# Optimization experiments

Measured on AMD Instinct MI355X. Metric: run time of the kernel, lower is better.

Reference implementation:

```python
import jax, jax.numpy as jnp
import numpy as np

N_NODES = 200000
D_FEAT = 128
B = 40000
DEG = 16
E = B * DEG
D_OUT = 256
N_CLASSES = 128


def setup_inputs() -> dict:
    key = jax.random.key(0)
    ks = jax.random.split(key, 8)
    inputs = jax.random.randint(ks[0], (B,), 0, N_NODES)
    neighbor_ids = jax.random.randint(ks[1], (E,), 0, N_NODES)
    segment_ids = jnp.repeat(jnp.arange(B, dtype=jnp.int64 if jax.config.jax_enable_x64 else jnp.int32), DEG)
    feat_data = jax.random.normal(ks[2], (N_NODES, D_FEAT), dtype=jnp.float32)
    W1 = jax.random.normal(ks[3], (D_OUT, 2 * D_FEAT), dtype=jnp.float32) * 0.05
    b1 = jax.random.normal(ks[4], (D_OUT,), dtype=jnp.float32) * 0.05
    W3 = jax.random.normal(ks[5], (N_CLASSES, D_OUT), dtype=jnp.float32) * 0.05
    b3 = jax.random.normal(ks[6], (N_CLASSES,), dtype=jnp.float32) * 0.05
    return {"inputs": inputs, "neighbor_ids": neighbor_ids, "segment_ids": segment_ids,
            "feat_data": feat_data, "W1": W1, "b1": b1, "W3": W3, "b3": b3}


def reference(inputs, neighbor_ids, segment_ids, feat_data, W1, b1, W3, b3):
    # Segment-mean over neighbor features (replaces Python per-node loop)
    neigh = feat_data[neighbor_ids]                               # [E, D]
    sums = jax.ops.segment_sum(neigh, segment_ids, num_segments=B)  # [B, D]
    cnt = jax.ops.segment_sum(jnp.ones((E,), jnp.float32), segment_ids, num_segments=B)
    means = sums / jnp.maximum(cnt, 1.0)[:, None]                 # [B, D]
    # Concat self + neighbor-mean, linear1
    emb = jnp.concatenate([feat_data[inputs], means], axis=1)     # [B, 2D]
    h = emb @ W1.T + b1                                           # [B, D_OUT]
    # ReLU -> linear3 -> L2 normalize (F.normalize, eps=1e-12)
    logits = jax.nn.relu(h) @ W3.T + b3                           # [B, n_classes]
    norm = jnp.linalg.norm(logits, axis=1, keepdims=True)
    return logits / jnp.maximum(norm, 1e-12)
```

## Files before the change

### kernel.cpp

```cpp
#include <hip/hip_runtime.h>
#include <stdint.h>

#define NNODES 200000
#define BNODES 40000
#define DEG    16
#define DFEAT  128
#define DOUT   256
#define NCLS   128
#define TILE   32

typedef __attribute__((ext_vector_type(8))) __bf16 bf16x8;
typedef __attribute__((ext_vector_type(4))) float  floatx4;

__device__ __forceinline__ uint32_t f2bf(float f) {
  uint32_t x = __float_as_uint(f);
  return ((x + 0x7fffu + ((x >> 16) & 1u)) >> 16) & 0xffffu;
}

__global__ void cvt_weights(const float* __restrict__ W1, const float* __restrict__ W3,
                            uint16_t* __restrict__ w1b, uint16_t* __restrict__ w3b) {
  int i = blockIdx.x * 256 + threadIdx.x;
  if (i < DOUT * 2 * DFEAT) w1b[i] = (uint16_t)f2bf(W1[i]);
  if (i < NCLS * DOUT)      w3b[i] = (uint16_t)f2bf(W3[i]);
}

__global__ __launch_bounds__(256) void sage_fused(
    const int* __restrict__ inputs, const int* __restrict__ nbr,
    const float* __restrict__ feat,
    const uint16_t* __restrict__ w1b, const float* __restrict__ b1,
    const uint16_t* __restrict__ w3b, const float* __restrict__ b3,
    float* __restrict__ out) {
  __shared__ __align__(16) uint16_t embL[TILE][264];
  __shared__ __align__(16) uint16_t hL[TILE][264];
  __shared__ __align__(16) float    lgL[TILE][132];

  const int tid  = threadIdx.x;
  const int w    = tid >> 6;
  const int lane = tid & 63;
  const int quad = lane >> 4;
  const int l16  = lane & 15;

  {
    const int nodeBase = blockIdx.x * TILE + w * 8;
#pragma unroll
    for (int n = 0; n < 8; ++n) {
      const int node = nodeBase + n;
      const int row  = w * 8 + n;
      const int* nb  = nbr + node * DEG;
      float sx = 0.f, sy = 0.f;
#pragma unroll
      for (int j = 0; j < DEG; ++j) {
        const float2 v = *(const float2*)(feat + (size_t)nb[j] * DFEAT + lane * 2);
        sx += v.x; sy += v.y;
      }
      const float2 sv = *(const float2*)(feat + (size_t)inputs[node] * DFEAT + lane * 2);
      const uint32_t selfp = f2bf(sv.x) | (f2bf(sv.y) << 16);
      const uint32_t meanp = f2bf(sx * 0.0625f) | (f2bf(sy * 0.0625f) << 16);
      *(uint32_t*)&embL[row][lane * 2]         = selfp;
      *(uint32_t*)&embL[row][DFEAT + lane * 2] = meanp;
    }
  }
  __syncthreads();

  const int kq = quad * 8;

  {
    floatx4 acc[2][4];
#pragma unroll
    for (int mt = 0; mt < 2; ++mt)
#pragma unroll
      for (int ot = 0; ot < 4; ++ot) {
        floatx4 z = {0.f, 0.f, 0.f, 0.f};
        acc[mt][ot] = z;
      }
#pragma unroll
    for (int kt = 0; kt < 8; ++kt) {
      const int k0 = kt * 32 + kq;
      const bf16x8 a0 = *(const bf16x8*)&embL[l16][k0];
      const bf16x8 a1 = *(const bf16x8*)&embL[16 + l16][k0];
#pragma unroll
      for (int ot = 0; ot < 4; ++ot) {
        const int o = (w * 4 + ot) * 16 + l16;
        const bf16x8 b = *(const bf16x8*)(w1b + o * 256 + k0);
        acc[0][ot] = __builtin_amdgcn_mfma_f32_16x16x32_bf16(a0, b, acc[0][ot], 0, 0, 0);
        acc[1][ot] = __builtin_amdgcn_mfma_f32_16x16x32_bf16(a1, b, acc[1][ot], 0, 0, 0);
      }
    }
#pragma unroll
    for (int ot = 0; ot < 4; ++ot) {
      const int o = (w * 4 + ot) * 16 + l16;
      const float bias = b1[o];
#pragma unroll
      for (int mt = 0; mt < 2; ++mt)
#pragma unroll
        for (int r = 0; r < 4; ++r) {
          float v = acc[mt][ot][r] + bias;
          v = fmaxf(v, 0.f);
          hL[mt * 16 + quad * 4 + r][o] = (uint16_t)f2bf(v);
        }
    }
  }
  __syncthreads();

  {
    floatx4 acc2[2][2];
#pragma unroll
    for (int mt = 0; mt < 2; ++mt)
#pragma unroll
      for (int ct = 0; ct < 2; ++ct) {
        floatx4 z = {0.f, 0.f, 0.f, 0.f};
        acc2[mt][ct] = z;
      }
#pragma unroll
    for (int kt = 0; kt < 8; ++kt) {
      const int k0 = kt * 32 + kq;
      const bf16x8 a0 = *(const bf16x8*)&hL[l16][k0];
      const bf16x8 a1 = *(const bf16x8*)&hL[16 + l16][k0];
#pragma unroll
      for (int ct = 0; ct < 2; ++ct) {
        const int c = (w * 2 + ct) * 16 + l16;
        const bf16x8 b = *(const bf16x8*)(w3b + c * 256 + k0);
        acc2[0][ct] = __builtin_amdgcn_mfma_f32_16x16x32_bf16(a0, b, acc2[0][ct], 0, 0, 0);
        acc2[1][ct] = __builtin_amdgcn_mfma_f32_16x16x32_bf16(a1, b, acc2[1][ct], 0, 0, 0);
      }
    }
#pragma unroll
    for (int ct = 0; ct < 2; ++ct) {
      const int c = (w * 2 + ct) * 16 + l16;
      const float bias = b3[c];
#pragma unroll
      for (int mt = 0; mt < 2; ++mt)
#pragma unroll
        for (int r = 0; r < 4; ++r)
          lgL[mt * 16 + quad * 4 + r][c] = acc2[mt][ct][r] + bias;
    }
  }
  __syncthreads();

  {
    const int nr  = tid >> 3;
    const int sub = tid & 7;
    const float* lrow = &lgL[nr][sub * 16];
    float4 v0 = *(const float4*)(lrow + 0);
    float4 v1 = *(const float4*)(lrow + 4);
    float4 v2 = *(const float4*)(lrow + 8);
    float4 v3 = *(const float4*)(lrow + 12);
    float ss = v0.x * v0.x + v0.y * v0.y + v0.z * v0.z + v0.w * v0.w
             + v1.x * v1.x + v1.y * v1.y + v1.z * v1.z + v1.w * v1.w
             + v2.x * v2.x + v2.y * v2.y + v2.z * v2.z + v2.w * v2.w
             + v3.x * v3.x + v3.y * v3.y + v3.z * v3.z + v3.w * v3.w;
    ss += __shfl_xor(ss, 1);
    ss += __shfl_xor(ss, 2);
    ss += __shfl_xor(ss, 4);
    const float scale = 1.f / fmaxf(sqrtf(ss), 1e-12f);
    v0.x *= scale; v0.y *= scale; v0.z *= scale; v0.w *= scale;
    v1.x *= scale; v1.y *= scale; v1.z *= scale; v1.w *= scale;
    v2.x *= scale; v2.y *= scale; v2.z *= scale; v2.w *= scale;
    v3.x *= scale; v3.y *= scale; v3.z *= scale; v3.w *= scale;
    float* op = out + ((size_t)(blockIdx.x * TILE + nr)) * NCLS + sub * 16;
    *(float4*)(op + 0)  = v0;
    *(float4*)(op + 4)  = v1;
    *(float4*)(op + 8)  = v2;
    *(float4*)(op + 12) = v3;
  }
}

extern "C" void kernel_launch(void* const* d_in, const int* in_sizes, int n_in,
                              void* d_out, int out_size, void* d_ws, size_t ws_size,
                              hipStream_t stream) {
  const int*   inputs = (const int*)d_in[0];
  const int*   nbr    = (const int*)d_in[1];
  const float* feat   = (const float*)d_in[3];
  const float* W1     = (const float*)d_in[4];
  const float* b1     = (const float*)d_in[5];
  const float* W3     = (const float*)d_in[6];
  const float* b3     = (const float*)d_in[7];

  uint16_t* w1b = (uint16_t*)d_ws;
  uint16_t* w3b = w1b + DOUT * 2 * DFEAT;

  cvt_weights<<<(DOUT * 2 * DFEAT) / 256, 256, 0, stream>>>(W1, W3, w1b, w3b);
  sage_fused<<<BNODES / TILE, 256, 0, stream>>>(inputs, nbr, feat, w1b, b1, w3b, b3,
                                                (float*)d_out);
}
```

Before: 218.0 us.

## Alias LDS buffers, widen gather loads to float4, raise occupancy hint

The embedding and logits staging buffers now share one LDS union, guarded by an extra barrier, which shrinks shared memory per block. The neighbor gather now uses float4 loads, with each half-wavefront handling alternate neighbors and a cross-half shuffle to combine the sums. Self features are loaded in a separate float4 pass. A launch-bounds hint of four blocks per CU is added so more waves stay resident to hide gather latency, at the cost of an extra barrier and possible register pressure.

```diff
diff --git a/kernel.cpp b/kernel.cpp
--- a/kernel.cpp
+++ b/kernel.cpp
@@ -24,15 +24,17 @@
   if (i < NCLS * DOUT)      w3b[i] = (uint16_t)f2bf(W3[i]);
 }
 
-__global__ __launch_bounds__(256) void sage_fused(
+__global__ __launch_bounds__(256, 4) void sage_fused(
     const int* __restrict__ inputs, const int* __restrict__ nbr,
     const float* __restrict__ feat,
     const uint16_t* __restrict__ w1b, const float* __restrict__ b1,
     const uint16_t* __restrict__ w3b, const float* __restrict__ b3,
     float* __restrict__ out) {
-  __shared__ __align__(16) uint16_t embL[TILE][264];
+  __shared__ __align__(16) union {
+    uint16_t emb[TILE][264];
+    float    lg[TILE][132];
+  } u0;
   __shared__ __align__(16) uint16_t hL[TILE][264];
-  __shared__ __align__(16) float    lgL[TILE][132];
 
   const int tid  = threadIdx.x;
   const int w    = tid >> 6;
@@ -41,23 +43,46 @@
   const int l16  = lane & 15;
 
   {
+    const int half = lane >> 5;
+    const int hl   = lane & 31;
     const int nodeBase = blockIdx.x * TILE + w * 8;
+
+#pragma unroll
+    for (int p = 0; p < 4; ++p) {
+      const int n0   = 2 * p + half;
+      const int node = nodeBase + n0;
+      const int row  = w * 8 + n0;
+      const float4 v = *(const float4*)(feat + (size_t)inputs[node] * DFEAT + hl * 4);
+      uint2 pk;
+      pk.x = f2bf(v.x) | (f2bf(v.y) << 16);
+      pk.y = f2bf(v.z) | (f2bf(v.w) << 16);
+      *(uint2*)&u0.emb[row][hl * 4] = pk;
+    }
+
 #pragma unroll
     for (int n = 0; n < 8; ++n) {
       const int node = nodeBase + n;
       const int row  = w * 8 + n;
       const int* nb  = nbr + node * DEG;
-      float sx = 0.f, sy = 0.f;
-#pragma unroll
-      for (int j = 0; j < DEG; ++j) {
-        const float2 v = *(const float2*)(feat + (size_t)nb[j] * DFEAT + lane * 2);
-        sx += v.x; sy += v.y;
-      }
-      const float2 sv = *(const float2*)(feat + (size_t)inputs[node] * DFEAT + lane * 2);
-      const uint32_t selfp = f2bf(sv.x) | (f2bf(sv.y) << 16);
-      const uint32_t meanp = f2bf(sx * 0.0625f) | (f2bf(sy * 0.0625f) << 16);
-      *(uint32_t*)&embL[row][lane * 2]         = selfp;
-      *(uint32_t*)&embL[row][DFEAT + lane * 2] = meanp;
+      float4 a = {0.f, 0.f, 0.f, 0.f};
+#pragma unroll
+      for (int j = 0; j < 8; ++j) {
+        const int i0 = nb[2 * j];
+        const int i1 = nb[2 * j + 1];
+        const int idx = half ? i1 : i0;
+        const float4 v = *(const float4*)(feat + (size_t)idx * DFEAT + hl * 4);
+        a.x += v.x; a.y += v.y; a.z += v.z; a.w += v.w;
+      }
+      a.x += __shfl_xor(a.x, 32);
+      a.y += __shfl_xor(a.y, 32);
+      a.z += __shfl_xor(a.z, 32);
+      a.w += __shfl_xor(a.w, 32);
+      if (half == 0) {
+        uint2 pk;
+        pk.x = f2bf(a.x * 0.0625f) | (f2bf(a.y * 0.0625f) << 16);
+        pk.y = f2bf(a.z * 0.0625f) | (f2bf(a.w * 0.0625f) << 16);
+        *(uint2*)&u0.emb[row][DFEAT + hl * 4] = pk;
+      }
     }
   }
   __syncthreads();
@@ -76,8 +101,8 @@
 #pragma unroll
     for (int kt = 0; kt < 8; ++kt) {
       const int k0 = kt * 32 + kq;
-      const bf16x8 a0 = *(const bf16x8*)&embL[l16][k0];
-      const bf16x8 a1 = *(const bf16x8*)&embL[16 + l16][k0];
+      const bf16x8 a0 = *(const bf16x8*)&u0.emb[l16][k0];
+      const bf16x8 a1 = *(const bf16x8*)&u0.emb[16 + l16][k0];
 #pragma unroll
       for (int ot = 0; ot < 4; ++ot) {
         const int o = (w * 4 + ot) * 16 + l16;
@@ -124,6 +149,7 @@
         acc2[1][ct] = __builtin_amdgcn_mfma_f32_16x16x32_bf16(a1, b, acc2[1][ct], 0, 0, 0);
       }
     }
+    __syncthreads();
 #pragma unroll
     for (int ct = 0; ct < 2; ++ct) {
       const int c = (w * 2 + ct) * 16 + l16;
@@ -132,7 +158,7 @@
       for (int mt = 0; mt < 2; ++mt)
 #pragma unroll
         for (int r = 0; r < 4; ++r)
-          lgL[mt * 16 + quad * 4 + r][c] = acc2[mt][ct][r] + bias;
+          u0.lg[mt * 16 + quad * 4 + r][c] = acc2[mt][ct][r] + bias;
     }
   }
   __syncthreads();
@@ -140,7 +166,7 @@
   {
     const int nr  = tid >> 3;
     const int sub = tid & 7;
-    const float* lrow = &lgL[nr][sub * 16];
+    const float* lrow = &u0.lg[nr][sub * 16];
     float4 v0 = *(const float4*)(lrow + 0);
     float4 v1 = *(const float4*)(lrow + 4);
     float4 v2 = *(const float4*)(lrow + 8);
```

New measurement: 218.7 us. About the same (+0.3%).

## Interleave neighbor gathers across nodes and alias logits LDS with embedding buffer

Applied to the files above, without the earlier changes.

The gather loop is reordered so each wave issues loads for all 8 nodes at each neighbor index, and self features are loaded up front. This raises the number of independent global loads in flight and so hides gather latency better. The logits buffer now shares LDS with the embedding buffer through a union, with an extra barrier before the write. That cuts shared memory per block, which may allow more blocks per CU, at the cost of more live registers and one more sync.

```diff
diff --git a/kernel.cpp b/kernel.cpp
--- a/kernel.cpp
+++ b/kernel.cpp
@@ -30,9 +30,11 @@
     const uint16_t* __restrict__ w1b, const float* __restrict__ b1,
     const uint16_t* __restrict__ w3b, const float* __restrict__ b3,
     float* __restrict__ out) {
-  __shared__ __align__(16) uint16_t embL[TILE][264];
+  __shared__ __align__(16) union {
+    uint16_t emb[TILE][264];
+    float    lg[TILE][132];
+  } u0;
   __shared__ __align__(16) uint16_t hL[TILE][264];
-  __shared__ __align__(16) float    lgL[TILE][132];
 
   const int tid  = threadIdx.x;
   const int w    = tid >> 6;
@@ -42,22 +44,33 @@
 
   {
     const int nodeBase = blockIdx.x * TILE + w * 8;
+    const int* nbp = nbr + nodeBase * DEG;
+
+    float2 sv[8];
+#pragma unroll
+    for (int n = 0; n < 8; ++n)
+      sv[n] = *(const float2*)(feat + (size_t)inputs[nodeBase + n] * DFEAT + lane * 2);
+
+    float2 acc[8];
+#pragma unroll
+    for (int n = 0; n < 8; ++n) { acc[n].x = 0.f; acc[n].y = 0.f; }
+
+#pragma unroll
+    for (int j = 0; j < DEG; ++j) {
+#pragma unroll
+      for (int n = 0; n < 8; ++n) {
+        const int idx = nbp[n * DEG + j];
+        const float2 v = *(const float2*)(feat + (size_t)idx * DFEAT + lane * 2);
+        acc[n].x += v.x; acc[n].y += v.y;
+      }
+    }
+
 #pragma unroll
     for (int n = 0; n < 8; ++n) {
-      const int node = nodeBase + n;
-      const int row  = w * 8 + n;
-      const int* nb  = nbr + node * DEG;
-      float sx = 0.f, sy = 0.f;
-#pragma unroll
-      for (int j = 0; j < DEG; ++j) {
-        const float2 v = *(const float2*)(feat + (size_t)nb[j] * DFEAT + lane * 2);
-        sx += v.x; sy += v.y;
-      }
-      const float2 sv = *(const float2*)(feat + (size_t)inputs[node] * DFEAT + lane * 2);
-      const uint32_t selfp = f2bf(sv.x) | (f2bf(sv.y) << 16);
-      const uint32_t meanp = f2bf(sx * 0.0625f) | (f2bf(sy * 0.0625f) << 16);
-      *(uint32_t*)&embL[row][lane * 2]         = selfp;
-      *(uint32_t*)&embL[row][DFEAT + lane * 2] = meanp;
+      const int row = w * 8 + n;
+      *(uint32_t*)&u0.emb[row][lane * 2] = f2bf(sv[n].x) | (f2bf(sv[n].y) << 16);
+      *(uint32_t*)&u0.emb[row][DFEAT + lane * 2] =
+          f2bf(acc[n].x * 0.0625f) | (f2bf(acc[n].y * 0.0625f) << 16);
     }
   }
   __syncthreads();
@@ -76,8 +89,8 @@
 #pragma unroll
     for (int kt = 0; kt < 8; ++kt) {
       const int k0 = kt * 32 + kq;
-      const bf16x8 a0 = *(const bf16x8*)&embL[l16][k0];
-      const bf16x8 a1 = *(const bf16x8*)&embL[16 + l16][k0];
+      const bf16x8 a0 = *(const bf16x8*)&u0.emb[l16][k0];
+      const bf16x8 a1 = *(const bf16x8*)&u0.emb[16 + l16][k0];
 #pragma unroll
       for (int ot = 0; ot < 4; ++ot) {
         const int o = (w * 4 + ot) * 16 + l16;
@@ -124,6 +137,7 @@
         acc2[1][ct] = __builtin_amdgcn_mfma_f32_16x16x32_bf16(a1, b, acc2[1][ct], 0, 0, 0);
       }
     }
+    __syncthreads();
 #pragma unroll
     for (int ct = 0; ct < 2; ++ct) {
       const int c = (w * 2 + ct) * 16 + l16;
@@ -132,7 +146,7 @@
       for (int mt = 0; mt < 2; ++mt)
 #pragma unroll
         for (int r = 0; r < 4; ++r)
-          lgL[mt * 16 + quad * 4 + r][c] = acc2[mt][ct][r] + bias;
+          u0.lg[mt * 16 + quad * 4 + r][c] = acc2[mt][ct][r] + bias;
     }
   }
   __syncthreads();
@@ -140,7 +154,7 @@
   {
     const int nr  = tid >> 3;
     const int sub = tid & 7;
-    const float* lrow = &lgL[nr][sub * 16];
+    const float* lrow = &u0.lg[nr][sub * 16];
     float4 v0 = *(const float4*)(lrow + 0);
     float4 v1 = *(const float4*)(lrow + 4);
     float4 v2 = *(const float4*)(lrow + 8);
```

Measured after the change: 223.4 us. 1.03x slower.
